# Optimization experiments

Hardware: AMD Instinct MI355X
Metric: run time of the kernel (lower is better)

The kernel has to match this reference:

```python
import jax, jax.numpy as jnp
import numpy as np

D_MODEL = 2048
HEADS = 2
DIM = 32


def setup_inputs() -> dict:
    key = jax.random.key(0)
    kx, kq, kk, kw = jax.random.split(key, 4)
    b, t = 2, 4096
    x = jax.random.normal(kx, (b, t, D_MODEL), dtype=jnp.float32)
    # Linear weights stored as [in, out] so forward is x @ W
    s = 1.0 / np.sqrt(D_MODEL)
    wq = jax.random.uniform(kq, (D_MODEL, HEADS * DIM), jnp.float32, -s, s)
    wk = jax.random.uniform(kk, (D_MODEL, DIM), jnp.float32, -s, s)
    ww = jax.random.uniform(kw, (D_MODEL, HEADS), jnp.float32, -s, s)
    return {"x": x, "wq": wq, "wk": wk, "ww": ww}


def reference(x, wq, wk, ww):
    b, t, _ = x.shape
    queries = (x @ wq).reshape(b, t, HEADS, DIM)   # [b,t,h,d]
    keys = x @ wk                                   # [b,s,d]
    weights = x @ ww                                # [b,t,h]
    dots = jnp.einsum('bthd,bsd->bths', queries, keys)  # [b,t,h,s]
    activated = jax.nn.relu(dots)
    # multiply by per-(t,h) weight and sum over heads in one contraction
    index_scores = jnp.einsum('bths,bth->bts', activated, weights)
    return index_scores
```

## Files before the change

### kernel.cpp

```cpp
#include <hip/hip_runtime.h>

#define D_MODEL 2048
#define T 4096
#define NBATCH 2
#define ROWS (NBATCH*T)

typedef __attribute__((ext_vector_type(4))) float f32x4;
typedef __attribute__((ext_vector_type(2))) float f32x2;
typedef __attribute__((ext_vector_type(4))) int   i32x4;
typedef __attribute__((ext_vector_type(8))) short bf16x8;

union FU { i32x4 i; bf16x8 b; };

__device__ __forceinline__ unsigned fbits(float v){ return __builtin_bit_cast(unsigned, v); }
__device__ __forceinline__ float bcastf(unsigned u){ return __builtin_bit_cast(float, u); }
__device__ __forceinline__ int pack_hi(float a, float b) {
  return (int)__builtin_amdgcn_perm(fbits(b), fbits(a), 0x07060302u);
}
__device__ __forceinline__ float resid(float v) {
  return v - bcastf(fbits(v) & 0xFFFF0000u);
}
__device__ __forceinline__ void cvt_frag(f32x4 v0, f32x4 v1, bf16x8& h, bf16x8& l) {
  FU H, L;
  H.i[0]=pack_hi(v0[0],v0[1]); H.i[1]=pack_hi(v0[2],v0[3]);
  H.i[2]=pack_hi(v1[0],v1[1]); H.i[3]=pack_hi(v1[2],v1[3]);
  L.i[0]=pack_hi(resid(v0[0]),resid(v0[1])); L.i[1]=pack_hi(resid(v0[2]),resid(v0[3]));
  L.i[2]=pack_hi(resid(v1[0]),resid(v1[1])); L.i[3]=pack_hi(resid(v1[2]),resid(v1[3]));
  h = H.b; l = L.b;
}
__device__ __forceinline__ f32x4 mfma16(bf16x8 a, bf16x8 b, f32x4 c) {
  return __builtin_amdgcn_mfma_f32_16x16x32_bf16(a, b, c, 0, 0, 0);
}

__global__ __launch_bounds__(256)
void wprep_kernel(const float* __restrict__ wq, const float* __restrict__ wk,
                  const float* __restrict__ ww, unsigned char* __restrict__ Wpk) {
  const int lane = threadIdx.x & 63;
  const int chunk = blockIdx.x * 4 + (threadIdx.x >> 6);
  const int ks = chunk / 7, nt = chunk % 7;
  const int col = nt*16 + (lane & 15);
  const int kb  = ks*32 + (lane >> 4)*8;
  float v[8];
  #pragma unroll
  for (int j = 0; j < 8; ++j) {
    int k = kb + j;
    float t;
    if      (col < 64) t = wq[(size_t)k*64 + col];
    else if (col < 96) t = wk[(size_t)k*32 + (col-64)];
    else if (col < 98) t = ww[(size_t)k*2  + (col-96)];
    else               t = 0.f;
    v[j] = t;
  }
  i32x4 hi = { pack_hi(v[0],v[1]), pack_hi(v[2],v[3]), pack_hi(v[4],v[5]), pack_hi(v[6],v[7]) };
  i32x4 lo = { pack_hi(resid(v[0]),resid(v[1])), pack_hi(resid(v[2]),resid(v[3])),
               pack_hi(resid(v[4]),resid(v[5])), pack_hi(resid(v[6]),resid(v[7])) };
  unsigned char* base = Wpk + ((size_t)chunk << 11) + lane*16;
  *(i32x4*)base          = hi;
  *(i32x4*)(base + 1024) = lo;
}

__global__ __launch_bounds__(512, 2)
void proj_kernel(const float* __restrict__ x, const unsigned char* __restrict__ Wpk,
                 unsigned short* __restrict__ Ppk, float* __restrict__ Pw) {
  const int tid = threadIdx.x, lane = tid & 63, wv = tid >> 6;
  const int l15 = lane & 15, kg = lane >> 4;
  const int mt = wv >> 2, wp = wv & 3;
  const int m0 = blockIdx.x * 32;
  const bool hasB = (wp < 3);
  const int ntA = wp, ntB = wp + 4;

  const float* xrow = x + (size_t)(m0 + mt*16 + l15) * D_MODEL + kg*8;
  f32x4 acc0 = {0,0,0,0}, acc1 = {0,0,0,0};

  #pragma unroll 4
  for (int ks = 0; ks < 64; ++ks) {
    f32x4 v0 = *(const f32x4*)(xrow + ks*32);
    f32x4 v1 = *(const f32x4*)(xrow + ks*32 + 4);
    bf16x8 ah, al; cvt_frag(v0, v1, ah, al);
    const unsigned char* cb = Wpk + (((size_t)ks*7 + ntA) << 11) + lane*16;
    FU bh, bl; bh.i = *(const i32x4*)cb; bl.i = *(const i32x4*)(cb + 1024);
    acc0 = mfma16(ah, bh.b, acc0);
    acc0 = mfma16(ah, bl.b, acc0);
    acc0 = mfma16(al, bh.b, acc0);
    if (hasB) {
      const unsigned char* cb2 = Wpk + (((size_t)ks*7 + ntB) << 11) + lane*16;
      FU bh2, bl2; bh2.i = *(const i32x4*)cb2; bl2.i = *(const i32x4*)(cb2 + 1024);
      acc1 = mfma16(ah, bh2.b, acc1);
      acc1 = mfma16(ah, bl2.b, acc1);
      acc1 = mfma16(al, bh2.b, acc1);
    }
  }
  #pragma unroll
  for (int s = 0; s < 2; ++s) {
    if (s == 1 && !hasB) break;
    const int nt = (s == 0) ? ntA : ntB;
    f32x4 a = (s == 0) ? acc0 : acc1;
    #pragma unroll
    for (int j = 0; j < 4; ++j) {
      const int row = m0 + mt*16 + kg*4 + j;
      const float v = a[j];
      if (nt < 6) {
        const int c = nt*16 + l15;
        unsigned u = fbits(v);
        Ppk[(size_t)row*192 + c]      = (unsigned short)(u >> 16);
        Ppk[(size_t)row*192 + 96 + c] = (unsigned short)(fbits(resid(v)) >> 16);
      } else if (l15 < 2) {
        Pw[(size_t)row*2 + l15] = v;
      }
    }
  }
}

__global__ __launch_bounds__(256, 4)
void score_kernel(const unsigned char* __restrict__ Ppk, const float* __restrict__ Pw,
                  float* __restrict__ out) {
  __shared__ float cbuf[4][16][76];
  const int tid = threadIdx.x, lane = tid & 63, wv = tid >> 6;
  const int l15 = lane & 15, kg = lane >> 4;
  const int wt = wv >> 1, wsi = wv & 1;
  const int bz = blockIdx.z;
  const int t0 = blockIdx.y * 128 + wt*64;
  const int s0 = blockIdx.x * 128 + wsi*64;
  const size_t rbase = (size_t)bz * T;

  bf16x8 bh[4], bl[4];
  #pragma unroll
  for (int nt = 0; nt < 4; ++nt) {
    const unsigned char* pb = Ppk + (rbase + s0 + nt*16 + l15)*384 + 128 + kg*16;
    FU h, l; h.i = *(const i32x4*)pb; l.i = *(const i32x4*)(pb + 192);
    bh[nt] = h.b; bl[nt] = l.b;
  }

  for (int mt = 0; mt < 4; ++mt) {
    bf16x8 ah[2], al[2];
    #pragma unroll
    for (int h = 0; h < 2; ++h) {
      const unsigned char* pa = Ppk + (rbase + t0 + mt*16 + l15)*384 + h*64 + kg*16;
      FU hh, ll; hh.i = *(const i32x4*)pa; ll.i = *(const i32x4*)(pa + 192);
      ah[h] = hh.b; al[h] = ll.b;
    }
    float w0[4], w1[4];
    #pragma unroll
    for (int j = 0; j < 4; ++j) {
      f32x2 w = *(const f32x2*)(Pw + (rbase + t0 + mt*16 + kg*4 + j)*2);
      w0[j] = w[0]; w1[j] = w[1];
    }
    #pragma unroll
    for (int nt = 0; nt < 4; ++nt) {
      f32x4 a0 = {0,0,0,0}, a1 = {0,0,0,0};
      a0 = mfma16(ah[0], bh[nt], a0);
      a0 = mfma16(ah[0], bl[nt], a0);
      a0 = mfma16(al[0], bh[nt], a0);
      a1 = mfma16(ah[1], bh[nt], a1);
      a1 = mfma16(ah[1], bl[nt], a1);
      a1 = mfma16(al[1], bh[nt], a1);
      #pragma unroll
      for (int j = 0; j < 4; ++j) {
        cbuf[wv][kg*4+j][nt*16 + l15] =
            fmaf(w0[j], fmaxf(a0[j], 0.f), w1[j] * fmaxf(a1[j], 0.f));
      }
    }
    __syncthreads();
    #pragma unroll
    for (int it = 0; it < 4; ++it) {
      const int r = it*4 + kg;
      f32x4 vv = *(const f32x4*)&cbuf[wv][r][l15*4];
      *(f32x4*)(out + (size_t)bz*T*T + (size_t)(t0 + mt*16 + r)*T + s0 + l15*4) = vv;
    }
    __syncthreads();
  }
}

extern "C" void kernel_launch(void* const* d_in, const int* in_sizes, int n_in,
                              void* d_out, int out_size, void* d_ws, size_t ws_size,
                              hipStream_t stream) {
  const float* x  = (const float*)d_in[0];
  const float* wq = (const float*)d_in[1];
  const float* wk = (const float*)d_in[2];
  const float* ww = (const float*)d_in[3];

  unsigned char*  Wpk = (unsigned char*)d_out;
  unsigned short* Ppk = (unsigned short*)d_ws;
  float*          Pw  = (float*)((unsigned char*)d_ws + (size_t)ROWS*384);
  float*          out = (float*)d_out;

  wprep_kernel<<<dim3(112), 256, 0, stream>>>(wq, wk, ww, Wpk);
  proj_kernel<<<dim3(ROWS/32), 512, 0, stream>>>(x, Wpk, Ppk, Pw);
  score_kernel<<<dim3(T/128, T/128, NBATCH), 256, 0, stream>>>(
      (const unsigned char*)Ppk, Pw, out);
}
```

Before: 260.8 us.

## Prefetch x tiles in registers, drop block barriers, use nontemporal output stores

```diff
diff --git a/kernel.cpp b/kernel.cpp
--- a/kernel.cpp
+++ b/kernel.cpp
@@ -72,24 +72,39 @@
   const float* xrow = x + (size_t)(m0 + mt*16 + l15) * D_MODEL + kg*8;
   f32x4 acc0 = {0,0,0,0}, acc1 = {0,0,0,0};
 
-  #pragma unroll 4
-  for (int ks = 0; ks < 64; ++ks) {
-    f32x4 v0 = *(const f32x4*)(xrow + ks*32);
-    f32x4 v1 = *(const f32x4*)(xrow + ks*32 + 4);
-    bf16x8 ah, al; cvt_frag(v0, v1, ah, al);
-    const unsigned char* cb = Wpk + (((size_t)ks*7 + ntA) << 11) + lane*16;
-    FU bh, bl; bh.i = *(const i32x4*)cb; bl.i = *(const i32x4*)(cb + 1024);
-    acc0 = mfma16(ah, bh.b, acc0);
-    acc0 = mfma16(ah, bl.b, acc0);
-    acc0 = mfma16(al, bh.b, acc0);
-    if (hasB) {
-      const unsigned char* cb2 = Wpk + (((size_t)ks*7 + ntB) << 11) + lane*16;
-      FU bh2, bl2; bh2.i = *(const i32x4*)cb2; bl2.i = *(const i32x4*)(cb2 + 1024);
-      acc1 = mfma16(ah, bh2.b, acc1);
-      acc1 = mfma16(ah, bl2.b, acc1);
-      acc1 = mfma16(al, bh2.b, acc1);
-    }
-  }
+  f32x4 cur[16], nxt[16];
+  #pragma unroll
+  for (int i = 0; i < 16; ++i)
+    cur[i] = *(const f32x4*)(xrow + (i >> 1)*32 + (i & 1)*4);
+
+  #pragma unroll 1
+  for (int g = 0; g < 8; ++g) {
+    if (g < 7) {
+      #pragma unroll
+      for (int i = 0; i < 16; ++i)
+        nxt[i] = *(const f32x4*)(xrow + (g+1)*256 + (i >> 1)*32 + (i & 1)*4);
+    }
+    #pragma unroll
+    for (int q = 0; q < 8; ++q) {
+      bf16x8 ah, al; cvt_frag(cur[2*q], cur[2*q+1], ah, al);
+      const size_t ks = (size_t)(g*8 + q);
+      const unsigned char* cb = Wpk + ((ks*7 + ntA) << 11) + lane*16;
+      FU bh, bl; bh.i = *(const i32x4*)cb; bl.i = *(const i32x4*)(cb + 1024);
+      acc0 = mfma16(ah, bh.b, acc0);
+      acc0 = mfma16(ah, bl.b, acc0);
+      acc0 = mfma16(al, bh.b, acc0);
+      if (hasB) {
+        const unsigned char* cb2 = Wpk + ((ks*7 + ntB) << 11) + lane*16;
+        FU bh2, bl2; bh2.i = *(const i32x4*)cb2; bl2.i = *(const i32x4*)(cb2 + 1024);
+        acc1 = mfma16(ah, bh2.b, acc1);
+        acc1 = mfma16(ah, bl2.b, acc1);
+        acc1 = mfma16(al, bh2.b, acc1);
+      }
+    }
+    #pragma unroll
+    for (int i = 0; i < 16; ++i) cur[i] = nxt[i];
+  }
+
   #pragma unroll
   for (int s = 0; s < 2; ++s) {
     if (s == 1 && !hasB) break;
@@ -101,8 +116,7 @@
       const float v = a[j];
       if (nt < 6) {
         const int c = nt*16 + l15;
-        unsigned u = fbits(v);
-        Ppk[(size_t)row*192 + c]      = (unsigned short)(u >> 16);
+        Ppk[(size_t)row*192 + c]      = (unsigned short)(fbits(v) >> 16);
         Ppk[(size_t)row*192 + 96 + c] = (unsigned short)(fbits(resid(v)) >> 16);
       } else if (l15 < 2) {
         Pw[(size_t)row*2 + l15] = v;
@@ -160,14 +174,13 @@
             fmaf(w0[j], fmaxf(a0[j], 0.f), w1[j] * fmaxf(a1[j], 0.f));
       }
     }
-    __syncthreads();
     #pragma unroll
     for (int it = 0; it < 4; ++it) {
       const int r = it*4 + kg;
       f32x4 vv = *(const f32x4*)&cbuf[wv][r][l15*4];
-      *(f32x4*)(out + (size_t)bz*T*T + (size_t)(t0 + mt*16 + r)*T + s0 + l15*4) = vv;
-    }
-    __syncthreads();
+      float* dst = out + (size_t)bz*T*T + (size_t)(t0 + mt*16 + r)*T + s0 + l15*4;
+      __builtin_nontemporal_store(vv, (f32x4*)dst);
+    }
   }
 }
 
```

Result: faster. 243.1 us (-6.8%).
